# Optimization experiments

Hardware: AMD Instinct MI355X
Metric: run time of the kernel (lower is better)

The kernel has to match this reference:

```python
import jax, jax.numpy as jnp
import numpy as np

VOCAB, HIDDEN, BATCH, SEQ = 50000, 256, 64, 2048


def setup_inputs() -> dict:
    key = jax.random.key(0)
    k1, k2, k3, k4 = jax.random.split(key, 4)
    embed = jax.random.normal(k1, (VOCAB, HIDDEN), dtype=jnp.float32) * 0.02
    embed = embed.at[0].set(0.0)  # padding_idx=0
    # orthogonal-ish init approximated by scaled normal; values irrelevant for correctness
    W_x_w = jax.random.normal(k2, (HIDDEN, HIDDEN), dtype=jnp.float32) / np.sqrt(HIDDEN)
    W_x_b = jnp.zeros((HIDDEN,), dtype=jnp.float32)
    W_h_w = jax.random.normal(k3, (HIDDEN, HIDDEN), dtype=jnp.float32) / np.sqrt(HIDDEN)
    x = jax.random.randint(k4, (BATCH, SEQ), 0, VOCAB)
    return {"x": x, "embed": embed, "W_x_w": W_x_w, "W_x_b": W_x_b, "W_h_w": W_h_w}


def reference(x, embed, W_x_w, W_x_b, W_h_w):
    # input projection precomputed for all timesteps: [B, S, H]
    inp = embed[x]                                  # embedding lookup (dropout p=0 is identity)
    x_pre = jnp.einsum('bsd,hd->bsh', inp, W_x_w) + W_x_b
    Wh_t = W_h_w.T                                  # matches torch.mm(h, W_h.weight.t())
    h0 = jnp.zeros((x.shape[0], W_h_w.shape[0]), dtype=x_pre.dtype)

    def step(h, xt):                                # xt: [B, H]
        h = jnp.tanh(xt + h @ Wh_t)
        return h, h

    _, all_states = jax.lax.scan(step, h0, jnp.swapaxes(x_pre, 0, 1))  # [S, B, H]
    return jnp.swapaxes(all_states, 0, 1)           # [B, S, H] (return_all_states=True)
```

## Files before the change

kernel.cpp:

```cpp
#include <hip/hip_runtime.h>
#include <hip/hip_bf16.h>

#define HIDDEN 256
#define BATCH  64
#define SEQ    2048

__global__ __launch_bounds__(256, 4)
void xpre_kernel(const int* __restrict__ x,
                 const float* __restrict__ embed,
                 const float* __restrict__ Wx,
                 const float* __restrict__ bias,
                 float* __restrict__ out) {
    const int tid = threadIdx.x;
    const int hh  = tid >> 7;
    const int j2  = tid & 127;
    const long row0 = (long)blockIdx.x * 32;

    __shared__ int toks[32];
    __shared__ __align__(16) float e[32][HIDDEN];

    if (tid < 32) toks[tid] = x[row0 + tid];
    __syncthreads();

    #pragma unroll
    for (int r = 0; r < 32; ++r) {
        e[r][tid] = embed[(long)toks[r] * HIDDEN + tid];
    }
    __syncthreads();

    float acc0[16], acc1[16];
    const float b0 = bias[j2];
    const float b1 = bias[j2 + 128];
    #pragma unroll
    for (int r = 0; r < 16; ++r) { acc0[r] = b0; acc1[r] = b1; }

    const float* wrow0 = Wx + (size_t)j2 * HIDDEN;
    const float* wrow1 = Wx + (size_t)(j2 + 128) * HIDDEN;

    #pragma unroll 2
    for (int d0 = 0; d0 < HIDDEN; d0 += 4) {
        const float4 w0 = *(const float4*)(wrow0 + d0);
        const float4 w1 = *(const float4*)(wrow1 + d0);
        #pragma unroll
        for (int r = 0; r < 16; ++r) {
            const float4 ev = *(const float4*)&e[(hh << 4) + r][d0];
            float a = acc0[r];
            a = fmaf(w0.x, ev.x, a); a = fmaf(w0.y, ev.y, a);
            a = fmaf(w0.z, ev.z, a); a = fmaf(w0.w, ev.w, a);
            acc0[r] = a;
            float c = acc1[r];
            c = fmaf(w1.x, ev.x, c); c = fmaf(w1.y, ev.y, c);
            c = fmaf(w1.z, ev.z, c); c = fmaf(w1.w, ev.w, c);
            acc1[r] = c;
        }
    }

    #pragma unroll
    for (int r = 0; r < 16; ++r) {
        const long orow = (row0 + (hh << 4) + r) * HIDDEN;
        out[orow + j2]       = acc0[r];
        out[orow + j2 + 128] = acc1[r];
    }
}


#define MAC_ASM(RD) \
  "ds_read_b128 v[48:51], " RD "\n\t" \
  "ds_read_b128 v[52:55], " RD " offset:16\n\t" \
  "ds_read_b128 v[56:59], " RD " offset:32\n\t" \
  "ds_read_b128 v[60:63], " RD " offset:48\n\t" \
  "s_waitcnt lgkmcnt(3)\n\t" \
  "v_pk_mul_f32 v[64:65], v[128:129], v[48:49]\n\t" \
  "v_pk_mul_f32 v[66:67], v[144:145], v[48:49]\n\t" \
  "v_pk_mul_f32 v[68:69], v[160:161], v[48:49]\n\t" \
  "v_pk_mul_f32 v[70:71], v[176:177], v[48:49]\n\t" \
  "v_pk_mul_f32 v[72:73], v[192:193], v[48:49]\n\t" \
  "v_pk_mul_f32 v[74:75], v[208:209], v[48:49]\n\t" \
  "v_pk_mul_f32 v[76:77], v[224:225], v[48:49]\n\t" \
  "v_pk_mul_f32 v[78:79], v[240:241], v[48:49]\n\t" \
  "v_pk_fma_f32 v[64:65], v[130:131], v[50:51], v[64:65]\n\t" \
  "v_pk_fma_f32 v[66:67], v[146:147], v[50:51], v[66:67]\n\t" \
  "v_pk_fma_f32 v[68:69], v[162:163], v[50:51], v[68:69]\n\t" \
  "v_pk_fma_f32 v[70:71], v[178:179], v[50:51], v[70:71]\n\t" \
  "v_pk_fma_f32 v[72:73], v[194:195], v[50:51], v[72:73]\n\t" \
  "v_pk_fma_f32 v[74:75], v[210:211], v[50:51], v[74:75]\n\t" \
  "v_pk_fma_f32 v[76:77], v[226:227], v[50:51], v[76:77]\n\t" \
  "v_pk_fma_f32 v[78:79], v[242:243], v[50:51], v[78:79]\n\t" \
  "s_waitcnt lgkmcnt(2)\n\t" \
  "v_pk_fma_f32 v[64:65], v[132:133], v[52:53], v[64:65]\n\t" \
  "v_pk_fma_f32 v[66:67], v[148:149], v[52:53], v[66:67]\n\t" \
  "v_pk_fma_f32 v[68:69], v[164:165], v[52:53], v[68:69]\n\t" \
  "v_pk_fma_f32 v[70:71], v[180:181], v[52:53], v[70:71]\n\t" \
  "v_pk_fma_f32 v[72:73], v[196:197], v[52:53], v[72:73]\n\t" \
  "v_pk_fma_f32 v[74:75], v[212:213], v[52:53], v[74:75]\n\t" \
  "v_pk_fma_f32 v[76:77], v[228:229], v[52:53], v[76:77]\n\t" \
  "v_pk_fma_f32 v[78:79], v[244:245], v[52:53], v[78:79]\n\t" \
  "v_pk_fma_f32 v[64:65], v[134:135], v[54:55], v[64:65]\n\t" \
  "v_pk_fma_f32 v[66:67], v[150:151], v[54:55], v[66:67]\n\t" \
  "v_pk_fma_f32 v[68:69], v[166:167], v[54:55], v[68:69]\n\t" \
  "v_pk_fma_f32 v[70:71], v[182:183], v[54:55], v[70:71]\n\t" \
  "v_pk_fma_f32 v[72:73], v[198:199], v[54:55], v[72:73]\n\t" \
  "v_pk_fma_f32 v[74:75], v[214:215], v[54:55], v[74:75]\n\t" \
  "v_pk_fma_f32 v[76:77], v[230:231], v[54:55], v[76:77]\n\t" \
  "v_pk_fma_f32 v[78:79], v[246:247], v[54:55], v[78:79]\n\t" \
  "s_waitcnt lgkmcnt(1)\n\t" \
  "v_pk_fma_f32 v[64:65], v[136:137], v[56:57], v[64:65]\n\t" \
  "v_pk_fma_f32 v[66:67], v[152:153], v[56:57], v[66:67]\n\t" \
  "v_pk_fma_f32 v[68:69], v[168:169], v[56:57], v[68:69]\n\t" \
  "v_pk_fma_f32 v[70:71], v[184:185], v[56:57], v[70:71]\n\t" \
  "v_pk_fma_f32 v[72:73], v[200:201], v[56:57], v[72:73]\n\t" \
  "v_pk_fma_f32 v[74:75], v[216:217], v[56:57], v[74:75]\n\t" \
  "v_pk_fma_f32 v[76:77], v[232:233], v[56:57], v[76:77]\n\t" \
  "v_pk_fma_f32 v[78:79], v[248:249], v[56:57], v[78:79]\n\t" \
  "v_pk_fma_f32 v[64:65], v[138:139], v[58:59], v[64:65]\n\t" \
  "v_pk_fma_f32 v[66:67], v[154:155], v[58:59], v[66:67]\n\t" \
  "v_pk_fma_f32 v[68:69], v[170:171], v[58:59], v[68:69]\n\t" \
  "v_pk_fma_f32 v[70:71], v[186:187], v[58:59], v[70:71]\n\t" \
  "v_pk_fma_f32 v[72:73], v[202:203], v[58:59], v[72:73]\n\t" \
  "v_pk_fma_f32 v[74:75], v[218:219], v[58:59], v[74:75]\n\t" \
  "v_pk_fma_f32 v[76:77], v[234:235], v[58:59], v[76:77]\n\t" \
  "v_pk_fma_f32 v[78:79], v[250:251], v[58:59], v[78:79]\n\t" \
  "s_waitcnt lgkmcnt(0)\n\t" \
  "v_pk_fma_f32 v[64:65], v[140:141], v[60:61], v[64:65]\n\t" \
  "v_pk_fma_f32 v[66:67], v[156:157], v[60:61], v[66:67]\n\t" \
  "v_pk_fma_f32 v[68:69], v[172:173], v[60:61], v[68:69]\n\t" \
  "v_pk_fma_f32 v[70:71], v[188:189], v[60:61], v[70:71]\n\t" \
  "v_pk_fma_f32 v[72:73], v[204:205], v[60:61], v[72:73]\n\t" \
  "v_pk_fma_f32 v[74:75], v[220:221], v[60:61], v[74:75]\n\t" \
  "v_pk_fma_f32 v[76:77], v[236:237], v[60:61], v[76:77]\n\t" \
  "v_pk_fma_f32 v[78:79], v[252:253], v[60:61], v[78:79]\n\t" \
  "v_pk_fma_f32 v[64:65], v[142:143], v[62:63], v[64:65]\n\t" \
  "v_pk_fma_f32 v[66:67], v[158:159], v[62:63], v[66:67]\n\t" \
  "v_pk_fma_f32 v[68:69], v[174:175], v[62:63], v[68:69]\n\t" \
  "v_pk_fma_f32 v[70:71], v[190:191], v[62:63], v[70:71]\n\t" \
  "v_pk_fma_f32 v[72:73], v[206:207], v[62:63], v[72:73]\n\t" \
  "v_pk_fma_f32 v[74:75], v[222:223], v[62:63], v[74:75]\n\t" \
  "v_pk_fma_f32 v[76:77], v[238:239], v[62:63], v[76:77]\n\t" \
  "v_pk_fma_f32 v[78:79], v[254:255], v[62:63], v[78:79]\n\t" \
  "v_add_f32 v80, v64, v65\n\t" \
  "v_add_f32 v81, v66, v67\n\t" \
  "v_add_f32 v82, v68, v69\n\t" \
  "v_add_f32 v83, v70, v71\n\t" \
  "v_add_f32 v84, v72, v73\n\t" \
  "v_add_f32 v85, v74, v75\n\t" \
  "v_add_f32 v86, v76, v77\n\t" \
  "v_add_f32 v87, v78, v79\n\t"

#define RED_ASM \
  "v_add_f32_dpp v80, v80, v80 row_ror:8 row_mask:0xf bank_mask:0xf\n\t" \
  "v_add_f32_dpp v81, v81, v81 row_ror:8 row_mask:0xf bank_mask:0xf\n\t" \
  "v_add_f32_dpp v82, v82, v82 row_ror:8 row_mask:0xf bank_mask:0xf\n\t" \
  "v_add_f32_dpp v83, v83, v83 row_ror:8 row_mask:0xf bank_mask:0xf\n\t" \
  "v_add_f32_dpp v84, v84, v84 row_ror:8 row_mask:0xf bank_mask:0xf\n\t" \
  "v_add_f32_dpp v85, v85, v85 row_ror:8 row_mask:0xf bank_mask:0xf\n\t" \
  "v_add_f32_dpp v86, v86, v86 row_ror:8 row_mask:0xf bank_mask:0xf\n\t" \
  "v_add_f32_dpp v87, v87, v87 row_ror:8 row_mask:0xf bank_mask:0xf\n\t" \
  "v_cndmask_b32 v88, v81, v80, s[24:25]\n\t" \
  "v_cndmask_b32 v89, v83, v82, s[24:25]\n\t" \
  "v_cndmask_b32 v90, v85, v84, s[24:25]\n\t" \
  "v_cndmask_b32 v91, v87, v86, s[24:25]\n\t" \
  "v_cndmask_b32 v80, v80, v81, s[24:25]\n\t" \
  "v_cndmask_b32 v82, v82, v83, s[24:25]\n\t" \
  "v_cndmask_b32 v84, v84, v85, s[24:25]\n\t" \
  "v_cndmask_b32 v86, v86, v87, s[24:25]\n\t" \
  "v_add_f32_dpp v80, v88, v80 quad_perm:[1,0,3,2] row_mask:0xf bank_mask:0xf\n\t" \
  "v_add_f32_dpp v82, v89, v82 quad_perm:[1,0,3,2] row_mask:0xf bank_mask:0xf\n\t" \
  "v_add_f32_dpp v84, v90, v84 quad_perm:[1,0,3,2] row_mask:0xf bank_mask:0xf\n\t" \
  "v_add_f32_dpp v86, v91, v86 quad_perm:[1,0,3,2] row_mask:0xf bank_mask:0xf\n\t" \
  "v_cndmask_b32 v88, v82, v80, s[26:27]\n\t" \
  "v_cndmask_b32 v89, v86, v84, s[26:27]\n\t" \
  "v_cndmask_b32 v80, v80, v82, s[26:27]\n\t" \
  "v_cndmask_b32 v84, v84, v86, s[26:27]\n\t" \
  "s_nop 1\n\t" \
  "v_add_f32_dpp v80, v88, v80 quad_perm:[2,3,0,1] row_mask:0xf bank_mask:0xf\n\t" \
  "v_add_f32_dpp v84, v89, v84 quad_perm:[2,3,0,1] row_mask:0xf bank_mask:0xf\n\t" \
  "v_cndmask_b32 v88, v84, v80, s[28:29]\n\t" \
  "v_cndmask_b32 v80, v80, v84, s[28:29]\n\t" \
  "s_nop 1\n\t" \
  "v_add_f32_dpp v80, v88, v80 row_ror:4 row_mask:0xf bank_mask:0xf\n\t"

#define FIN_ASM(WR, XP, MD, MS) \
  "s_waitcnt vmcnt(2)\n\t" \
  "v_add_f32 v99, v80, " XP "\n\t" \
  "v_mul_f32 v93, 0x4038AA3B, v99\n\t" \
  "v_exp_f32 v94, v93\n\t" \
  "s_nop 0\n\t" \
  "v_add_f32 v94, 1.0, v94\n\t" \
  "v_rcp_f32 v95, v94\n\t" \
  "s_nop 0\n\t" \
  "v_fma_f32 v99, -2.0, v95, v96\n\t" \
  "s_and_saveexec_b64 s[20:21], s[22:23]\n\t" \
  "ds_write_b32 " WR ", v99\n\t" \
  "global_store_dword v[100:101], v99, off offset:-2048\n\t" \
  "s_mov_b64 exec, s[20:21]\n\t" \
  "v_mov_b32 " MD ", " MS "\n\t" \
  "v_add_co_u32 v100, vcc, 0x400, v100\n\t" \
  "v_addc_co_u32 v101, vcc, v101, 0, vcc\n\t" \
  "s_waitcnt lgkmcnt(0)\n\t" \
  "s_barrier\n\t"

__global__ __attribute__((amdgpu_flat_work_group_size(512, 512)))
void rnn_scan_kernel(const float* __restrict__ Wh,
                     float* __restrict__ out) {
    const int tid = threadIdx.x;
    const int o   = tid & 15;
    const int pc  = tid >> 4;
    const int b   = blockIdx.x;

    __shared__ __align__(16) float hraw[1024];
    hraw[tid] = 0.0f; hraw[tid + 512] = 0.0f;
    __syncthreads();

    unsigned lbase = (unsigned)(unsigned long long)
                     (__attribute__((address_space(3))) char*)hraw;
    const int col  = pc + 32 * (o & 7);
    const int slot = col + 4 * (col >> 4);
    const unsigned rda = lbase + 80u * (unsigned)o;
    const unsigned rdb = rda + 2048u;
    const unsigned wra = lbase + 2048u + 4u * (unsigned)slot;
    const unsigned wrb = wra - 2048u;

    const float* xa = out + ((size_t)b * SEQ + 2) * HIDDEN + col;
    const unsigned xlo = (unsigned)(size_t)xa;
    const unsigned xhi = (unsigned)((size_t)xa >> 32);

    const float* wp0 = Wh + (size_t)(pc +   0) * HIDDEN + 16 * o;
    const float* wp1 = Wh + (size_t)(pc +  32) * HIDDEN + 16 * o;
    const float* wp2 = Wh + (size_t)(pc +  64) * HIDDEN + 16 * o;
    const float* wp3 = Wh + (size_t)(pc +  96) * HIDDEN + 16 * o;
    const float* wp4 = Wh + (size_t)(pc + 128) * HIDDEN + 16 * o;
    const float* wp5 = Wh + (size_t)(pc + 160) * HIDDEN + 16 * o;
    const float* wp6 = Wh + (size_t)(pc + 192) * HIDDEN + 16 * o;
    const float* wp7 = Wh + (size_t)(pc + 224) * HIDDEN + 16 * o;

    asm volatile(
        "v_mov_b32 v100, %[xlo]\n\t"
        "v_mov_b32 v101, %[xhi]\n\t"
        "v_mov_b32 v96, 1.0\n\t"
        "global_load_dwordx4 v[128:131], %[wp0], off\n\t"
        "global_load_dwordx4 v[132:135], %[wp0], off offset:16\n\t"
        "global_load_dwordx4 v[136:139], %[wp0], off offset:32\n\t"
        "global_load_dwordx4 v[140:143], %[wp0], off offset:48\n\t"
        "global_load_dwordx4 v[144:147], %[wp1], off\n\t"
        "global_load_dwordx4 v[148:151], %[wp1], off offset:16\n\t"
        "global_load_dwordx4 v[152:155], %[wp1], off offset:32\n\t"
        "global_load_dwordx4 v[156:159], %[wp1], off offset:48\n\t"
        "global_load_dwordx4 v[160:163], %[wp2], off\n\t"
        "global_load_dwordx4 v[164:167], %[wp2], off offset:16\n\t"
        "global_load_dwordx4 v[168:171], %[wp2], off offset:32\n\t"
        "global_load_dwordx4 v[172:175], %[wp2], off offset:48\n\t"
        "global_load_dwordx4 v[176:179], %[wp3], off\n\t"
        "global_load_dwordx4 v[180:183], %[wp3], off offset:16\n\t"
        "global_load_dwordx4 v[184:187], %[wp3], off offset:32\n\t"
        "global_load_dwordx4 v[188:191], %[wp3], off offset:48\n\t"
        "global_load_dwordx4 v[192:195], %[wp4], off\n\t"
        "global_load_dwordx4 v[196:199], %[wp4], off offset:16\n\t"
        "global_load_dwordx4 v[200:203], %[wp4], off offset:32\n\t"
        "global_load_dwordx4 v[204:207], %[wp4], off offset:48\n\t"
        "global_load_dwordx4 v[208:211], %[wp5], off\n\t"
        "global_load_dwordx4 v[212:215], %[wp5], off offset:16\n\t"
        "global_load_dwordx4 v[216:219], %[wp5], off offset:32\n\t"
        "global_load_dwordx4 v[220:223], %[wp5], off offset:48\n\t"
        "global_load_dwordx4 v[224:227], %[wp6], off\n\t"
        "global_load_dwordx4 v[228:231], %[wp6], off offset:16\n\t"
        "global_load_dwordx4 v[232:235], %[wp6], off offset:32\n\t"
        "global_load_dwordx4 v[236:239], %[wp6], off offset:48\n\t"
        "global_load_dwordx4 v[240:243], %[wp7], off\n\t"
        "global_load_dwordx4 v[244:247], %[wp7], off offset:16\n\t"
        "global_load_dwordx4 v[248:251], %[wp7], off offset:32\n\t"
        "global_load_dwordx4 v[252:255], %[wp7], off offset:48\n\t"
        "global_load_dword v97,  v[100:101], off offset:-2048\n\t"
        "global_load_dword v103, v[100:101], off offset:-1024\n\t"
        "v_and_b32 v88, 1, %[vo]\n\t"
        "v_cmp_eq_u32 s[24:25], 1, v88\n\t"
        "v_and_b32 v88, 2, %[vo]\n\t"
        "v_cmp_eq_u32 s[26:27], 2, v88\n\t"
        "v_and_b32 v88, 4, %[vo]\n\t"
        "v_cmp_eq_u32 s[28:29], 4, v88\n\t"
        "v_cmp_gt_u32 s[22:23], 8, %[vo]\n\t"
        "s_movk_i32 s30, 0x400\n\t"
        "s_waitcnt vmcnt(0)\n\t"
        "RNN%=:\n\t"
        "s_cmp_eq_u32 s30, 1\n\t"
        "s_cbranch_scc1 LDA%=\n\t"
        "global_load_dword v102, v[100:101], off\n\t"
        "s_branch LCA%=\n\t"
        "LDA%=:\n\t"
        "global_load_dword v102, v[100:101], off offset:-1024\n\t"
        "LCA%=:\n\t"
        MAC_ASM("%[rda]")
        RED_ASM
        FIN_ASM("%[wra]", "v97", "v98", "v103")
        "s_cmp_eq_u32 s30, 1\n\t"
        "s_cbranch_scc1 LDB%=\n\t"
        "global_load_dword v103, v[100:101], off\n\t"
        "s_branch LCB%=\n\t"
        "LDB%=:\n\t"
        "global_load_dword v103, v[100:101], off offset:-2048\n\t"
        "LCB%=:\n\t"
        MAC_ASM("%[rdb]")
        RED_ASM
        FIN_ASM("%[wrb]", "v98", "v97", "v102")
        "s_sub_u32 s30, s30, 1\n\t"
        "s_cmp_lg_u32 s30, 0\n\t"
        "s_cbranch_scc1 RNN%=\n\t"
        "s_waitcnt vmcnt(0) lgkmcnt(0)\n\t"
        :
        : [wp0] "v"(wp0), [wp1] "v"(wp1), [wp2] "v"(wp2), [wp3] "v"(wp3),
          [wp4] "v"(wp4), [wp5] "v"(wp5), [wp6] "v"(wp6), [wp7] "v"(wp7),
          [xlo] "v"(xlo), [xhi] "v"(xhi),
          [rda] "v"(rda), [rdb] "v"(rdb), [wra] "v"(wra), [wrb] "v"(wrb),
          [vo]  "v"(o)
        : "memory", "vcc", "scc",
          "s20","s21","s22","s23","s24","s25","s26","s27","s28","s29","s30",
          "v48","v49","v50","v51","v52","v53","v54","v55",
          "v56","v57","v58","v59","v60","v61","v62","v63",
          "v64","v65","v66","v67","v68","v69","v70","v71",
          "v72","v73","v74","v75","v76","v77","v78","v79",
          "v80","v81","v82","v83","v84","v85","v86","v87",
          "v88","v89","v90","v91","v92","v93","v94","v95",
          "v96","v97","v98","v99","v100","v101","v102","v103",
          "v104","v105","v106","v107","v108","v109","v110","v111",
          "v112","v113","v114","v115","v116","v117","v118","v119",
          "v120","v121","v122","v123","v124","v125","v126","v127",
          "v128","v129","v130","v131","v132","v133","v134","v135",
          "v136","v137","v138","v139","v140","v141","v142","v143",
          "v144","v145","v146","v147","v148","v149","v150","v151",
          "v152","v153","v154","v155","v156","v157","v158","v159",
          "v160","v161","v162","v163","v164","v165","v166","v167",
          "v168","v169","v170","v171","v172","v173","v174","v175",
          "v176","v177","v178","v179","v180","v181","v182","v183",
          "v184","v185","v186","v187","v188","v189","v190","v191",
          "v192","v193","v194","v195","v196","v197","v198","v199",
          "v200","v201","v202","v203","v204","v205","v206","v207",
          "v208","v209","v210","v211","v212","v213","v214","v215",
          "v216","v217","v218","v219","v220","v221","v222","v223",
          "v224","v225","v226","v227","v228","v229","v230","v231",
          "v232","v233","v234","v235","v236","v237","v238","v239",
          "v240","v241","v242","v243","v244","v245","v246","v247",
          "v248","v249","v250","v251","v252","v253","v254","v255");
}

extern "C" void kernel_launch(void* const* d_in, const int* in_sizes, int n_in,
                              void* d_out, int out_size, void* d_ws, size_t ws_size,
                              hipStream_t stream) {
    const int*   x     = (const int*)d_in[0];
    const float* embed = (const float*)d_in[1];
    const float* Wx    = (const float*)d_in[2];
    const float* Wxb   = (const float*)d_in[3];
    const float* Wh    = (const float*)d_in[4];
    float* out = (float*)d_out;

    const int nrows = BATCH * SEQ;
    xpre_kernel<<<nrows / 32, 256, 0, stream>>>(x, embed, Wx, Wxb, out);

    rnn_scan_kernel<<<BATCH, 512, 0, stream>>>(Wh, out);
}
```

Measured before the change: 1.372 ms.

## Read embedding rows directly via scalar loads instead of staging in LDS

The xpre kernel no longer copies the 32 gathered embedding rows into shared memory. Each thread now computes one output column for all 32 rows and reads embedding values straight from global memory through wave-uniform pointers (readfirstlane), which lets the compiler use scalar loads. This drops the LDS staging, its barrier and the per-row ds_reads. In exchange each thread holds 32 accumulators plus 32 row pointers, raising register pressure, and scalar-cache behaviour on the gathered rows is uncertain. The xpre kernel is probably a small share of the total time next to the sequential recurrence.

```diff
diff --git a/kernel.cpp b/kernel.cpp
--- a/kernel.cpp
+++ b/kernel.cpp
@@ -12,54 +12,44 @@
                  const float* __restrict__ bias,
                  float* __restrict__ out) {
     const int tid = threadIdx.x;
-    const int hh  = tid >> 7;
-    const int j2  = tid & 127;
     const long row0 = (long)blockIdx.x * 32;
 
     __shared__ int toks[32];
-    __shared__ __align__(16) float e[32][HIDDEN];
-
     if (tid < 32) toks[tid] = x[row0 + tid];
     __syncthreads();
 
+    const float* erow[32];
     #pragma unroll
     for (int r = 0; r < 32; ++r) {
-        e[r][tid] = embed[(long)toks[r] * HIDDEN + tid];
+        const int tok = __builtin_amdgcn_readfirstlane(toks[r]);
+        erow[r] = embed + (size_t)tok * HIDDEN;
     }
-    __syncthreads();
-
-    float acc0[16], acc1[16];
-    const float b0 = bias[j2];
-    const float b1 = bias[j2 + 128];
+
+    float acc[32];
+    const float bj = bias[tid];
     #pragma unroll
-    for (int r = 0; r < 16; ++r) { acc0[r] = b0; acc1[r] = b1; }
-
-    const float* wrow0 = Wx + (size_t)j2 * HIDDEN;
-    const float* wrow1 = Wx + (size_t)(j2 + 128) * HIDDEN;
-
-    #pragma unroll 2
+    for (int r = 0; r < 32; ++r) acc[r] = bj;
+
+    const float* wrow = Wx + (size_t)tid * HIDDEN;
+
+    #pragma unroll 4
     for (int d0 = 0; d0 < HIDDEN; d0 += 4) {
-        const float4 w0 = *(const float4*)(wrow0 + d0);
-        const float4 w1 = *(const float4*)(wrow1 + d0);
+        const float4 w = *(const float4*)(wrow + d0);
         #pragma unroll
-        for (int r = 0; r < 16; ++r) {
-            const float4 ev = *(const float4*)&e[(hh << 4) + r][d0];
-            float a = acc0[r];
-            a = fmaf(w0.x, ev.x, a); a = fmaf(w0.y, ev.y, a);
-            a = fmaf(w0.z, ev.z, a); a = fmaf(w0.w, ev.w, a);
-            acc0[r] = a;
-            float c = acc1[r];
-            c = fmaf(w1.x, ev.x, c); c = fmaf(w1.y, ev.y, c);
-            c = fmaf(w1.z, ev.z, c); c = fmaf(w1.w, ev.w, c);
-            acc1[r] = c;
+        for (int r = 0; r < 32; ++r) {
+            const float4 ev = *(const float4*)(erow[r] + d0);
+            float a = acc[r];
+            a = fmaf(w.x, ev.x, a);
+            a = fmaf(w.y, ev.y, a);
+            a = fmaf(w.z, ev.z, a);
+            a = fmaf(w.w, ev.w, a);
+            acc[r] = a;
         }
     }
 
     #pragma unroll
-    for (int r = 0; r < 16; ++r) {
-        const long orow = (row0 + (hh << 4) + r) * HIDDEN;
-        out[orow + j2]       = acc0[r];
-        out[orow + j2 + 128] = acc1[r];
+    for (int r = 0; r < 32; ++r) {
+        out[(row0 + r) * HIDDEN + tid] = acc[r];
     }
 }
 
```

After: 1.703 ms. 24.1% more time.
